# Kernel optimization log

Hardware: AMD Instinct MI355X
Metric: run time of the kernel (lower is better)

## Reference

```python
import jax, jax.numpy as jnp
import numpy as np

HIDDEN = 1024
INTER = 4096


def setup_inputs() -> dict:
    key = jax.random.key(0)
    k1, k2, k3, k4, k5 = jax.random.split(key, 5)
    hidden_states = jax.random.normal(k1, (4, 4096, HIDDEN), dtype=jnp.float32)
    # nn.Linear stores weight as [out, in]; we keep that convention.
    W1 = jax.random.normal(k2, (INTER, HIDDEN), dtype=jnp.float32) * (1.0 / np.sqrt(HIDDEN))
    b1 = jax.random.normal(k3, (INTER,), dtype=jnp.float32) * 0.01
    W2 = jax.random.normal(k4, (HIDDEN, INTER), dtype=jnp.float32) * (1.0 / np.sqrt(INTER))
    b2 = jax.random.normal(k5, (HIDDEN,), dtype=jnp.float32) * 0.01
    return {"hidden_states": hidden_states, "W1": W1, "b1": b1, "W2": W2, "b2": b2}


def reference(hidden_states, W1, b1, W2, b2):
    # secure_matmul(x, W.T) + secure_add(bias)  ->  x @ W1.T + b1
    inter = jnp.einsum('bsh,fh->bsf', hidden_states, W1) + b1
    # secure_relu
    act = jax.nn.relu(inter)
    # second secure linear projection
    out = jnp.einsum('bsf,hf->bsh', act, W2) + b2
    return out
```

## Files before the change

### kernel.cpp

```cpp
#include <hip/hip_runtime.h>
#include <cstdint>
#include <cstddef>


typedef __bf16 bf16x8 __attribute__((ext_vector_type(8)));
typedef float f32x4 __attribute__((ext_vector_type(4)));

__device__ __forceinline__ unsigned short f32_to_bf16_rn(float f) {
  union { float f; unsigned int u; } v; v.f = f;
  unsigned int u = v.u;
  u += 0x7fffu + ((u >> 16) & 1u);
  return (unsigned short)(u >> 16);
}

__global__ void cvt_all(const float* __restrict__ x,
                        const float* __restrict__ w1,
                        const float* __restrict__ w2,
                        unsigned short* __restrict__ xb,
                        unsigned short* __restrict__ w1b,
                        unsigned short* __restrict__ w2b,
                        int nx4, int nw4) {
  const int stride = gridDim.x * blockDim.x;
  int i = blockIdx.x * blockDim.x + threadIdx.x;
  const int total = nx4 + 2 * nw4;
  for (; i < total; i += stride) {
    const float* src; unsigned short* dst; int j;
    if (i < nx4) { src = x; dst = xb; j = i; }
    else if (i < nx4 + nw4) { src = w1; dst = w1b; j = i - nx4; }
    else { src = w2; dst = w2b; j = i - nx4 - nw4; }
    const float4 v = reinterpret_cast<const float4*>(src)[j];
    ushort4 o;
    o.x = f32_to_bf16_rn(v.x);
    o.y = f32_to_bf16_rn(v.y);
    o.z = f32_to_bf16_rn(v.z);
    o.w = f32_to_bf16_rn(v.w);
    reinterpret_cast<ushort4*>(dst)[j] = o;
  }
}

__device__ __forceinline__ void gload_lds16(const void* g, void* l) {
  __builtin_amdgcn_global_load_lds(
      (const __attribute__((address_space(1))) void*)g,
      (__attribute__((address_space(3))) void*)l,
      16, 0, 0);
}

#define VMCNT6 asm volatile("s_waitcnt vmcnt(6)" ::: "memory")
#define VMCNT0 asm volatile("s_waitcnt vmcnt(0)" ::: "memory")
#define LGKMCNT0 asm volatile("s_waitcnt lgkmcnt(0)" ::: "memory")

#define APL(BUF, KH) (((BUF)*2 + (KH)) * 16384)
#define BPL(BUF, KH) (65536 + ((BUF)*2 + (KH)) * 16384)

#define STAGE(PLANEOFF, GROW, KB) do {                                          \
    gload_lds16((GROW) + (size_t)srow0 * pitch + (KB) + scol0,                  \
                lds + (PLANEOFF) + ldsw0);                                      \
    gload_lds16((GROW) + (size_t)srow1 * pitch + (KB) + scol1,                  \
                lds + (PLANEOFF) + ldsw1);                                      \
  } while (0)

#define PHASE(BUF, QK, QN, LOADA, STAGE_STMT, DOVM) do {                        \
    const unsigned char* pA_ = lds + APL(BUF, QK) + wroff + alane;              \
    const unsigned char* pB_ = lds + BPL(BUF, QK) + wcoff + alane;              \
    bfr[0] = *(const bf16x8*)(pB_ + (((QN)*2 + 0) << 10));                      \
    bfr[1] = *(const bf16x8*)(pB_ + (((QN)*2 + 1) << 10));                      \
    if (LOADA) {                                                                \
      _Pragma("unroll") for (int m_ = 0; m_ < 8; ++m_)                          \
        af[m_] = *(const bf16x8*)(pA_ + (m_ << 10));                            \
    }                                                                           \
    STAGE_STMT;                                                                 \
    __builtin_amdgcn_sched_barrier(0);                                          \
    __builtin_amdgcn_s_barrier();                                               \
    __builtin_amdgcn_sched_barrier(0);                                          \
    __builtin_amdgcn_s_setprio(1);                                              \
    _Pragma("unroll") for (int m_ = 0; m_ < 8; ++m_) {                          \
      acc[m_][(QN)*2 + 0] = __builtin_amdgcn_mfma_f32_16x16x32_bf16(            \
          af[m_], bfr[0], acc[m_][(QN)*2 + 0], 0, 0, 0);                        \
      acc[m_][(QN)*2 + 1] = __builtin_amdgcn_mfma_f32_16x16x32_bf16(            \
          af[m_], bfr[1], acc[m_][(QN)*2 + 1], 0, 0, 0);                        \
    }                                                                           \
    __builtin_amdgcn_s_setprio(0);                                              \
    if (DOVM) { VMCNT6; }                                                       \
    __builtin_amdgcn_sched_barrier(0);                                          \
    __builtin_amdgcn_s_barrier();                                               \
  } while (0)

template <int RELU_BF16_OUT, int NBN>
__global__ __launch_bounds__(512, 2) void gemm8(
    const unsigned short* __restrict__ A,
    const unsigned short* __restrict__ B,
    const float* __restrict__ bias,
    void* __restrict__ Cout,
    int K) {
  constexpr int N = NBN * 256;
  __shared__ unsigned char lds[131072];

  const int tid = threadIdx.x;
  const int l = tid & 63;
  const int w = tid >> 6;
  const int wr = w >> 2;
  const int wc = w & 3;

  const int nwg = gridDim.x;
  const int cpx = nwg >> 3;
  const int bid = blockIdx.x;
  const int swz = (bid & 7) * cpx + (bid >> 3);
  const int bmi = swz / NBN;
  const int bni = swz % NBN;

  const size_t pitch = (size_t)K * 2;
  const char* Ag = (const char*)A + (size_t)(bmi << 8) * pitch;
  const char* Bg = (const char*)B + (size_t)(bni << 8) * pitch;

  const int sd0 = tid << 4;
  const int sd1 = sd0 + 8192;
  const int srow0 = sd0 >> 6;
  const int srow1 = sd1 >> 6;
  const int scol0 = (sd0 & 63) ^ (((sd0 >> 7) & 3) << 4);
  const int scol1 = (sd1 & 63) ^ (((sd1 >> 7) & 3) << 4);
  const int ldsw0 = (w << 10);
  const int ldsw1 = 8192 + (w << 10);

  const int alane = ((l & 15) << 6) + (((l >> 4) << 4) ^ (((l >> 1) & 3) << 4));
  const int wroff = wr << 13;
  const int wcoff = wc << 12;

  f32x4 acc[8][4];
#pragma unroll
  for (int m = 0; m < 8; ++m)
#pragma unroll
    for (int n = 0; n < 4; ++n) { f32x4 z = 0.f; acc[m][n] = z; }
  bf16x8 af[8];
  bf16x8 bfr[2];

  const int nt = K >> 6;

  STAGE(APL(0, 0), Ag, 0);
  STAGE(BPL(0, 0), Bg, 0);
  STAGE(APL(0, 1), Ag, 64);
  STAGE(BPL(0, 1), Bg, 64);
  STAGE(APL(1, 0), Ag, 128);
  STAGE(BPL(1, 0), Bg, 128);
  STAGE(APL(1, 1), Ag, 192);
  VMCNT6;
  __builtin_amdgcn_s_barrier();

  for (int it = 0; it < (nt >> 1); ++it) {
    const int t1 = 2 * it + 1;
    int t2 = 2 * it + 2; if (t2 >= nt) t2 = nt - 1;
    int t3 = 2 * it + 3; if (t3 >= nt) t3 = nt - 1;
    const int kb1 = t1 << 7;
    const int kb2 = t2 << 7;
    const int kb3 = t3 << 7;

    PHASE(0, 0, 0, 1, STAGE(BPL(1, 1), Bg, kb1 + 64), 0);
    PHASE(0, 0, 1, 0, STAGE(APL(0, 0), Ag, kb2), 1);
    PHASE(0, 1, 0, 1, STAGE(BPL(0, 0), Bg, kb2), 0);
    PHASE(0, 1, 1, 0, STAGE(APL(0, 1), Ag, kb2 + 64), 1);
    PHASE(1, 0, 0, 1, STAGE(BPL(0, 1), Bg, kb2 + 64), 0);
    PHASE(1, 0, 1, 0, STAGE(APL(1, 0), Ag, kb3), 1);
    PHASE(1, 1, 0, 1, STAGE(BPL(1, 0), Bg, kb3), 0);
    PHASE(1, 1, 1, 0, STAGE(APL(1, 1), Ag, kb3 + 64), 1);
  }

  const int crow0 = (bmi << 8) + (wr << 7) + ((l >> 4) << 2);
  const int ccol0 = (bni << 8) + (wc << 6) + (l & 15);

  if (RELU_BF16_OUT) {
    VMCNT0;
    __builtin_amdgcn_s_barrier();
    float bv[4];
#pragma unroll
    for (int n = 0; n < 4; ++n) bv[n] = bias[ccol0 + (n << 4)];
    unsigned short* C = (unsigned short*)Cout;
    unsigned char* myl = lds + w * 9216;
    const int lw = l & 15;
    const int lg = l >> 4;
    for (int mp = 0; mp < 4; ++mp) {
#pragma unroll
      for (int m2 = 0; m2 < 2; ++m2) {
        const int m = mp * 2 + m2;
#pragma unroll
        for (int n = 0; n < 4; ++n) {
#pragma unroll
          for (int r = 0; r < 4; ++r) {
            const float v = fmaxf(acc[m][n][r] + bv[n], 0.0f);
            const int row = m2 * 16 + lg * 4 + r;
            *(float*)(myl + row * 288 + ((n * 16 + lw) << 2)) = v;
          }
        }
      }
      LGKMCNT0;
      __builtin_amdgcn_sched_barrier(0);
#pragma unroll
      for (int k = 0; k < 8; ++k) {
        const int row = k * 4 + lg;
        const float4 t = *(const float4*)(myl + row * 288 + (lw << 4));
        ushort4 o;
        o.x = f32_to_bf16_rn(t.x);
        o.y = f32_to_bf16_rn(t.y);
        o.z = f32_to_bf16_rn(t.z);
        o.w = f32_to_bf16_rn(t.w);
        const int grow = (bmi << 8) + (wr << 7) + (mp << 5) + row;
        const int gcol = (bni << 8) + (wc << 6) + (lw << 2);
        *(ushort4*)(C + (size_t)grow * N + gcol) = o;
      }
      LGKMCNT0;
      __builtin_amdgcn_sched_barrier(0);
    }
  } else {
    float* C = (float*)Cout;
#pragma unroll
    for (int n = 0; n < 4; ++n) {
      const int col = ccol0 + (n << 4);
      const float bv = bias[col];
#pragma unroll
      for (int m = 0; m < 8; ++m) {
#pragma unroll
        for (int r = 0; r < 4; ++r) {
          C[(size_t)(crow0 + (m << 4) + r) * N + col] = acc[m][n][r] + bv;
        }
      }
    }
  }
}

extern "C" void kernel_launch(void* const* d_in, const int* in_sizes, int n_in,
                              void* d_out, int out_size, void* d_ws, size_t ws_size,
                              hipStream_t stream) {
  const float* x  = (const float*)d_in[0];
  const float* W1 = (const float*)d_in[1];
  const float* b1 = (const float*)d_in[2];
  const float* W2 = (const float*)d_in[3];
  const float* b2 = (const float*)d_in[4];
  float* out = (float*)d_out;

  const int M = 16384, H = 1024, F = 4096;

  unsigned short* xb  = (unsigned short*)d_ws;
  unsigned short* w1b = xb + (size_t)M * H;
  unsigned short* w2b = w1b + (size_t)F * H;
  unsigned short* act = w2b + (size_t)H * F;

  cvt_all<<<2048, 256, 0, stream>>>(x, W1, W2, xb, w1b, w2b,
                                    (M * H) / 4, (F * H) / 4);

  gemm8<1, 16><<<dim3((M / 256) * (F / 256)), 512, 0, stream>>>(xb, w1b, b1, act, H);
  gemm8<0, 4><<<dim3((M / 256) * (H / 256)), 512, 0, stream>>>(act, w2b, b2, out, F);
}
```

Measured before the change: 395.5 us.

## Switch GEMM inner loop to 32x32x16 MFMA with reworked k-step pipeline

Replaces the 16x16x32 bf16 MFMA tiling (8x4 accumulators of 4 floats) with 32x32x16 MFMA (4x2 accumulators of 16 floats). The LDS fragment addressing and swizzle change to match, and the per-phase staging order is rescheduled with a deeper vmcnt wait. Each phase now loads 6 fragments instead of up to 10, which is meant to cut LDS read traffic and raise MFMA efficiency per instruction. The LDS-transposed bf16 epilogue is dropped in favour of direct scalar stores, which may hurt store coalescing for the intermediate activation.

```diff
diff --git a/kernel.cpp b/kernel.cpp
--- a/kernel.cpp
+++ b/kernel.cpp
@@ -4,7 +4,7 @@
 
 
 typedef __bf16 bf16x8 __attribute__((ext_vector_type(8)));
-typedef float f32x4 __attribute__((ext_vector_type(4)));
+typedef float f32x16 __attribute__((ext_vector_type(16)));
 
 __device__ __forceinline__ unsigned short f32_to_bf16_rn(float f) {
   union { float f; unsigned int u; } v; v.f = f;
@@ -45,9 +45,8 @@
       16, 0, 0);
 }
 
-#define VMCNT6 asm volatile("s_waitcnt vmcnt(6)" ::: "memory")
+#define VMCNT8 asm volatile("s_waitcnt vmcnt(8)" ::: "memory")
 #define VMCNT0 asm volatile("s_waitcnt vmcnt(0)" ::: "memory")
-#define LGKMCNT0 asm volatile("s_waitcnt lgkmcnt(0)" ::: "memory")
 
 #define APL(BUF, KH) (((BUF)*2 + (KH)) * 16384)
 #define BPL(BUF, KH) (65536 + ((BUF)*2 + (KH)) * 16384)
@@ -59,28 +58,28 @@
                 lds + (PLANEOFF) + ldsw1);                                      \
   } while (0)
 
-#define PHASE(BUF, QK, QN, LOADA, STAGE_STMT, DOVM) do {                        \
-    const unsigned char* pA_ = lds + APL(BUF, QK) + wroff + alane;              \
-    const unsigned char* pB_ = lds + BPL(BUF, QK) + wcoff + alane;              \
-    bfr[0] = *(const bf16x8*)(pB_ + (((QN)*2 + 0) << 10));                      \
-    bfr[1] = *(const bf16x8*)(pB_ + (((QN)*2 + 1) << 10));                      \
-    if (LOADA) {                                                                \
-      _Pragma("unroll") for (int m_ = 0; m_ < 8; ++m_)                          \
-        af[m_] = *(const bf16x8*)(pA_ + (m_ << 10));                            \
-    }                                                                           \
+#define PHASE(BUF, KST, STAGE_STMT, DOVM) do {                                  \
+    const unsigned char* pA_ =                                                  \
+        lds + APL(BUF, (KST) >> 1) + wroff + lrow64 + ach[(KST) & 1];           \
+    const unsigned char* pB_ =                                                  \
+        lds + BPL(BUF, (KST) >> 1) + wcoff + lrow64 + ach[(KST) & 1];           \
+    _Pragma("unroll") for (int mb_ = 0; mb_ < 4; ++mb_)                         \
+      a_[mb_] = *(const bf16x8*)(pA_ + (mb_ << 11));                            \
+    b_[0] = *(const bf16x8*)(pB_);                                              \
+    b_[1] = *(const bf16x8*)(pB_ + 2048);                                       \
     STAGE_STMT;                                                                 \
     __builtin_amdgcn_sched_barrier(0);                                          \
     __builtin_amdgcn_s_barrier();                                               \
     __builtin_amdgcn_sched_barrier(0);                                          \
     __builtin_amdgcn_s_setprio(1);                                              \
-    _Pragma("unroll") for (int m_ = 0; m_ < 8; ++m_) {                          \
-      acc[m_][(QN)*2 + 0] = __builtin_amdgcn_mfma_f32_16x16x32_bf16(            \
-          af[m_], bfr[0], acc[m_][(QN)*2 + 0], 0, 0, 0);                        \
-      acc[m_][(QN)*2 + 1] = __builtin_amdgcn_mfma_f32_16x16x32_bf16(            \
-          af[m_], bfr[1], acc[m_][(QN)*2 + 1], 0, 0, 0);                        \
+    _Pragma("unroll") for (int mb_ = 0; mb_ < 4; ++mb_) {                       \
+      acc[mb_][0] = __builtin_amdgcn_mfma_f32_32x32x16_bf16(                    \
+          a_[mb_], b_[0], acc[mb_][0], 0, 0, 0);                                \
+      acc[mb_][1] = __builtin_amdgcn_mfma_f32_32x32x16_bf16(                    \
+          a_[mb_], b_[1], acc[mb_][1], 0, 0, 0);                                \
     }                                                                           \
     __builtin_amdgcn_s_setprio(0);                                              \
-    if (DOVM) { VMCNT6; }                                                       \
+    if (DOVM) { VMCNT8; }                                                       \
     __builtin_amdgcn_sched_barrier(0);                                          \
     __builtin_amdgcn_s_barrier();                                               \
   } while (0)
@@ -121,17 +120,21 @@
   const int ldsw0 = (w << 10);
   const int ldsw1 = 8192 + (w << 10);
 
-  const int alane = ((l & 15) << 6) + (((l >> 4) << 4) ^ (((l >> 1) & 3) << 4));
+  const int lrow64 = (l & 31) << 6;
+  const int sxor = (l >> 1) & 3;
+  int ach[2];
+  ach[0] = ((0 * 2 + (l >> 5)) ^ sxor) << 4;
+  ach[1] = ((1 * 2 + (l >> 5)) ^ sxor) << 4;
   const int wroff = wr << 13;
   const int wcoff = wc << 12;
 
-  f32x4 acc[8][4];
-#pragma unroll
-  for (int m = 0; m < 8; ++m)
-#pragma unroll
-    for (int n = 0; n < 4; ++n) { f32x4 z = 0.f; acc[m][n] = z; }
-  bf16x8 af[8];
-  bf16x8 bfr[2];
+  f32x16 acc[4][2];
+#pragma unroll
+  for (int mb = 0; mb < 4; ++mb)
+#pragma unroll
+    for (int nb = 0; nb < 2; ++nb) { f32x16 z = 0.f; acc[mb][nb] = z; }
+  bf16x8 a_[4];
+  bf16x8 b_[2];
 
   const int nt = K >> 6;
 
@@ -141,8 +144,7 @@
   STAGE(BPL(0, 1), Bg, 64);
   STAGE(APL(1, 0), Ag, 128);
   STAGE(BPL(1, 0), Bg, 128);
-  STAGE(APL(1, 1), Ag, 192);
-  VMCNT6;
+  VMCNT8;
   __builtin_amdgcn_s_barrier();
 
   for (int it = 0; it < (nt >> 1); ++it) {
@@ -153,76 +155,56 @@
     const int kb2 = t2 << 7;
     const int kb3 = t3 << 7;
 
-    PHASE(0, 0, 0, 1, STAGE(BPL(1, 1), Bg, kb1 + 64), 0);
-    PHASE(0, 0, 1, 0, STAGE(APL(0, 0), Ag, kb2), 1);
-    PHASE(0, 1, 0, 1, STAGE(BPL(0, 0), Bg, kb2), 0);
-    PHASE(0, 1, 1, 0, STAGE(APL(0, 1), Ag, kb2 + 64), 1);
-    PHASE(1, 0, 0, 1, STAGE(BPL(0, 1), Bg, kb2 + 64), 0);
-    PHASE(1, 0, 1, 0, STAGE(APL(1, 0), Ag, kb3), 1);
-    PHASE(1, 1, 0, 1, STAGE(BPL(1, 0), Bg, kb3), 0);
-    PHASE(1, 1, 1, 0, STAGE(APL(1, 1), Ag, kb3 + 64), 1);
+    PHASE(0, 0, STAGE(APL(1, 1), Ag, kb1 + 64), 0);
+    PHASE(0, 1, STAGE(BPL(1, 1), Bg, kb1 + 64), 1);
+    PHASE(0, 2, STAGE(APL(0, 0), Ag, kb2), 0);
+    PHASE(0, 3, STAGE(BPL(0, 0), Bg, kb2), 1);
+    PHASE(1, 0, STAGE(APL(0, 1), Ag, kb2 + 64), 0);
+    PHASE(1, 1, STAGE(BPL(0, 1), Bg, kb2 + 64), 1);
+    PHASE(1, 2, STAGE(APL(1, 0), Ag, kb3), 0);
+    PHASE(1, 3, STAGE(BPL(1, 0), Bg, kb3), 1);
   }
 
-  const int crow0 = (bmi << 8) + (wr << 7) + ((l >> 4) << 2);
-  const int ccol0 = (bni << 8) + (wc << 6) + (l & 15);
+  const int crow_b = (bmi << 8) + (wr << 7) + ((l >> 5) << 2);
+  const int ccol_b = (bni << 8) + (wc << 6) + (l & 31);
 
   if (RELU_BF16_OUT) {
-    VMCNT0;
-    __builtin_amdgcn_s_barrier();
-    float bv[4];
-#pragma unroll
-    for (int n = 0; n < 4; ++n) bv[n] = bias[ccol0 + (n << 4)];
     unsigned short* C = (unsigned short*)Cout;
-    unsigned char* myl = lds + w * 9216;
-    const int lw = l & 15;
-    const int lg = l >> 4;
-    for (int mp = 0; mp < 4; ++mp) {
-#pragma unroll
-      for (int m2 = 0; m2 < 2; ++m2) {
-        const int m = mp * 2 + m2;
-#pragma unroll
-        for (int n = 0; n < 4; ++n) {
-#pragma unroll
-          for (int r = 0; r < 4; ++r) {
-            const float v = fmaxf(acc[m][n][r] + bv[n], 0.0f);
-            const int row = m2 * 16 + lg * 4 + r;
-            *(float*)(myl + row * 288 + ((n * 16 + lw) << 2)) = v;
-          }
+    float bv[2];
+    bv[0] = bias[ccol_b];
+    bv[1] = bias[ccol_b + 32];
+#pragma unroll
+    for (int mb = 0; mb < 4; ++mb) {
+#pragma unroll
+      for (int nb = 0; nb < 2; ++nb) {
+        const int col = ccol_b + (nb << 5);
+#pragma unroll
+        for (int reg = 0; reg < 16; ++reg) {
+          const int row = crow_b + (mb << 5) + (reg & 3) + ((reg >> 2) << 3);
+          const float v = fmaxf(acc[mb][nb][reg] + bv[nb], 0.0f);
+          C[(size_t)row * N + col] = f32_to_bf16_rn(v);
         }
       }
-      LGKMCNT0;
-      __builtin_amdgcn_sched_barrier(0);
-#pragma unroll
-      for (int k = 0; k < 8; ++k) {
-        const int row = k * 4 + lg;
-        const float4 t = *(const float4*)(myl + row * 288 + (lw << 4));
-        ushort4 o;
-        o.x = f32_to_bf16_rn(t.x);
-        o.y = f32_to_bf16_rn(t.y);
-        o.z = f32_to_bf16_rn(t.z);
-        o.w = f32_to_bf16_rn(t.w);
-        const int grow = (bmi << 8) + (wr << 7) + (mp << 5) + row;
-        const int gcol = (bni << 8) + (wc << 6) + (lw << 2);
-        *(ushort4*)(C + (size_t)grow * N + gcol) = o;
-      }
-      LGKMCNT0;
-      __builtin_amdgcn_sched_barrier(0);
     }
   } else {
     float* C = (float*)Cout;
-#pragma unroll
-    for (int n = 0; n < 4; ++n) {
-      const int col = ccol0 + (n << 4);
-      const float bv = bias[col];
-#pragma unroll
-      for (int m = 0; m < 8; ++m) {
-#pragma unroll
-        for (int r = 0; r < 4; ++r) {
-          C[(size_t)(crow0 + (m << 4) + r) * N + col] = acc[m][n][r] + bv;
+    float bv[2];
+    bv[0] = bias[ccol_b];
+    bv[1] = bias[ccol_b + 32];
+#pragma unroll
+    for (int mb = 0; mb < 4; ++mb) {
+#pragma unroll
+      for (int nb = 0; nb < 2; ++nb) {
+        const int col = ccol_b + (nb << 5);
+#pragma unroll
+        for (int reg = 0; reg < 16; ++reg) {
+          const int row = crow_b + (mb << 5) + (reg & 3) + ((reg >> 2) << 3);
+          C[(size_t)row * N + col] = acc[mb][nb][reg] + bv[nb];
         }
       }
     }
   }
+  VMCNT0;
 }
 
 extern "C" void kernel_launch(void* const* d_in, const int* in_sizes, int n_in,
```

Result: slower. 411.7 us (+4.1%).
